# Performance work log

Hardware: AMD Instinct MI355X
Metric: run time of the kernel (lower is better)

Reference implementation:

```python
import jax, jax.numpy as jnp
import numpy as np

B, N, C = 8, 8192, 256
H, D, S = 8, 32, 32          # heads, dim_head, slice_num
HID = 4 * C                  # mlp hidden


def layernorm(x, w, b, eps=1e-5):
    mu = jnp.mean(x, axis=-1, keepdims=True)
    var = jnp.mean(jnp.square(x - mu), axis=-1, keepdims=True)
    return (x - mu) * jax.lax.rsqrt(var + eps) * w + b


def setup_inputs() -> dict:
    key = jax.random.key(0)
    ks = jax.random.split(key, 16)
    s = lambda fan: 1.0 / np.sqrt(fan)
    return {
        "fx": jax.random.normal(ks[0], (B, N, C), jnp.float32),
        "ln1_w": jnp.ones((C,), jnp.float32),
        "ln1_b": jnp.zeros((C,), jnp.float32),
        "Wx": jax.random.uniform(ks[1], (C, C), jnp.float32, -s(C), s(C)),   # in_project_x weight [inner,dim]
        "bx": jax.random.uniform(ks[2], (C,), jnp.float32, -s(C), s(C)),
        "Wq": jax.random.uniform(ks[3], (S, D), jnp.float32, -s(D), s(D)),
        "Wk": jax.random.uniform(ks[4], (S, D), jnp.float32, -s(D), s(D)),
        "Wv": jax.random.uniform(ks[5], (D, D), jnp.float32, -s(D), s(D)),
        "Wo": jax.random.uniform(ks[6], (C, C), jnp.float32, -s(C), s(C)),   # to_out weight [dim,inner]
        "bo": jax.random.uniform(ks[7], (C,), jnp.float32, -s(C), s(C)),
        "ln2_w": jnp.ones((C,), jnp.float32),
        "ln2_b": jnp.zeros((C,), jnp.float32),
        "W1": jax.random.uniform(ks[8], (HID, C), jnp.float32, -s(C), s(C)),
        "b1": jax.random.uniform(ks[9], (HID,), jnp.float32, -s(C), s(C)),
        "W2": jax.random.uniform(ks[10], (C, HID), jnp.float32, -s(HID), s(HID)),
        "b2": jax.random.uniform(ks[11], (C,), jnp.float32, -s(HID), s(HID)),
    }


def linear_no_attn(x, Wx, bx, Wq, Wk, Wv, Wo, bo):
    # x: [B,N,C]
    x_mid = x @ Wx.T + bx                                   # [B,N,C]
    x_mid = x_mid.reshape(x.shape[0], x.shape[1], H, D).transpose(0, 2, 1, 3)  # [B,H,N,D]
    q = jax.nn.softmax(x_mid @ Wq.T, axis=-1)               # [B,H,N,S], softmax over slices
    k = jax.nn.softmax(x_mid @ Wk.T, axis=-2)               # [B,H,N,S], softmax over tokens
    v = x_mid @ Wv.T                                        # [B,H,N,D]
    kv = jnp.einsum('bhns,bhnd->bhsd', k, v)                # [B,H,S,D]
    qkv = jnp.einsum('bhns,bhsd->bhnd', q, kv)              # [B,H,N,D]
    qkv = qkv.transpose(0, 2, 1, 3).reshape(x.shape[0], x.shape[1], H * D)
    return qkv @ Wo.T + bo


def reference(fx, ln1_w, ln1_b, Wx, bx, Wq, Wk, Wv, Wo, bo, ln2_w, ln2_b, W1, b1, W2, b2):
    h = linear_no_attn(layernorm(fx, ln1_w, ln1_b), Wx, bx, Wq, Wk, Wv, Wo, bo) + fx
    y = layernorm(h, ln2_w, ln2_b)
    y = jax.nn.gelu(y @ W1.T + b1, approximate=False)       # MLP: pre + exact GELU, n_layers=0
    y = y @ W2.T + b2
    return y + h
```

## Files before the change

kernel.cpp:

```cpp
#include <hip/hip_runtime.h>
#include <math.h>


typedef __attribute__((ext_vector_type(8))) short bf8;
typedef __attribute__((ext_vector_type(4))) float f32x4;
typedef __attribute__((ext_vector_type(4))) unsigned short u16x4;
typedef __attribute__((ext_vector_type(8))) unsigned short u16x8;

__device__ __forceinline__ float b2f(unsigned short x) {
  union { unsigned u; float f; } t; t.u = ((unsigned)x) << 16; return t.f;
}
__device__ __forceinline__ unsigned short f2b(float f) {
  union { float f; unsigned u; } t; t.f = f;
  unsigned r = t.u + 0x7fffu + ((t.u >> 16) & 1u);
  return (unsigned short)(r >> 16);
}
__device__ __forceinline__ float gelu_exact(float x) {
  return 0.5f * x * (1.0f + erff(x * 0.7071067811865475f));
}
__device__ __forceinline__ float erf_fast(float x) {
  float ax = fabsf(x);
  float t = __builtin_amdgcn_rcpf(fmaf(0.3275911f, ax, 1.0f));
  float p = t * fmaf(t, fmaf(t, fmaf(t, fmaf(t, 1.061405429f, -1.453152027f),
                                     1.421413741f), -0.284496736f), 0.254829592f);
  float r = 1.0f - p * __expf(-ax * ax);
  return copysignf(r, x);
}
__device__ __forceinline__ float gelu_fast(float x) {
  return 0.5f * x * (1.0f + erf_fast(x * 0.7071067811865475f));
}

typedef __attribute__((address_space(1))) const void gas_void;
typedef __attribute__((address_space(3))) void las_void;
__device__ __forceinline__ void gl_lds16(const void* g, void* l) {
  __builtin_amdgcn_global_load_lds((gas_void*)g, (las_void*)l, 16, 0, 0);
}

__global__ void sniff_kernel(const unsigned* __restrict__ fx, int* __restrict__ flag) {
  if (threadIdx.x == 0) {
    int cnt = 0;
    for (int i = 0; i < 64; i++) {
      unsigned e = (fx[i] >> 7) & 0xFFu;
      cnt += (e >= 117u && e <= 130u) ? 1 : 0;
    }
    *flag = (cnt >= 32) ? 1 : 0;
  }
}

struct CvtDesc { const void* src[15]; int off[15]; int n[15]; };

__global__ __launch_bounds__(256) void cvt_tab(CvtDesc d, unsigned short* __restrict__ wtab,
                                               const int* __restrict__ flagp) {
  const int seg = blockIdx.y;
  const int i = blockIdx.x * 256 + threadIdx.x;
  if (i >= d.n[seg]) return;
  unsigned short o;
  if (*flagp) o = ((const unsigned short*)d.src[seg])[i];
  else        o = f2b(((const float*)d.src[seg])[i]);
  wtab[d.off[seg] + i] = o;
}

__global__ __launch_bounds__(256) void build_big(
    const unsigned short* __restrict__ wq, const unsigned short* __restrict__ wk,
    unsigned short* __restrict__ Wqbig, unsigned short* __restrict__ Wkbig)
{
  const int idx = blockIdx.x * 256 + threadIdx.x;
  const int row = idx >> 8, col = idx & 255;
  const bool same = (row >> 5) == (col >> 5);
  const int wi = (row & 31) * 32 + (col & 31);
  Wqbig[idx] = same ? wq[wi] : (unsigned short)0;
  Wkbig[idx] = same ? wk[wi] : (unsigned short)0;
}

__global__ __launch_bounds__(256) void zero_u16(unsigned short* __restrict__ p, int n) {
  int i8 = (blockIdx.x * 256 + threadIdx.x) * 8;
  if (i8 < n) { u16x8 z = {}; *(u16x8*)&p[i8] = z; }
}

__global__ __launch_bounds__(256) void ln_stats(
    const void* __restrict__ X, const int* __restrict__ flagp, int amode,
    float* __restrict__ MU, float* __restrict__ RS)
{
  const int lane = threadIdx.x & 63;
  const int wave = threadIdx.x >> 6;
  const size_t row = (size_t)blockIdx.x * 4 + wave;
  const size_t base = row * 256 + lane * 4;
  const bool abf = amode ? ((*flagp) != 0) : true;
  float x0, x1, x2, x3;
  if (abf) {
    u16x4 uv = *(const u16x4*)&((const unsigned short*)X)[base];
    x0 = b2f(uv[0]); x1 = b2f(uv[1]); x2 = b2f(uv[2]); x3 = b2f(uv[3]);
  } else {
    f32x4 t = *(const f32x4*)&((const float*)X)[base];
    x0 = t[0]; x1 = t[1]; x2 = t[2]; x3 = t[3];
  }
  float s = x0 + x1 + x2 + x3;
  float q = x0*x0 + x1*x1 + x2*x2 + x3*x3;
  #pragma unroll
  for (int m = 1; m < 64; m <<= 1) { s += __shfl_xor(s, m, 64); q += __shfl_xor(q, m, 64); }
  float mean = s * (1.0f / 256.0f);
  float var  = q * (1.0f / 256.0f) - mean * mean;
  if (lane == 0) { MU[row] = mean; RS[row] = rsqrtf(var + 1e-5f); }
}

__global__ __launch_bounds__(256) void gemm_bt(
    const unsigned short* __restrict__ A,
    const unsigned short* __restrict__ W,
    const unsigned short* __restrict__ bias,
    const void* __restrict__ Res, const int* __restrict__ flagp,
    unsigned short* __restrict__ Y,
    int N, int K, int act, int mz, long wz)
{
  __shared__ __align__(16) unsigned short smem[3 * 8192];
  const int tid = threadIdx.x, lane = tid & 63, wave = tid >> 6;
  const size_t zrow = (size_t)blockIdx.z * mz;
  const int bm = blockIdx.x * 128, bn = blockIdx.y * 128;
  const int wm = (wave >> 1) * 64, wn = (wave & 1) * 64;
  const int quad = lane >> 4, l16 = lane & 15;
  const unsigned short* Wz = W + (size_t)blockIdx.z * wz;

  f32x4 acc[4][4] = {};
  const int r0 = tid >> 2;
  const int co = (tid & 3) * 8;
  const unsigned short* pa0 = &A[(zrow + bm + r0) * K + co];
  const unsigned short* pa1 = &A[(zrow + bm + r0 + 64) * K + co];
  const unsigned short* pb0 = &Wz[(size_t)(bn + r0) * K + co];
  const unsigned short* pb1 = &Wz[(size_t)(bn + r0 + 64) * K + co];
  const int nt = K >> 5;

  auto stage = [&](int t, int sl) {
    const int k0 = t << 5;
    unsigned short* b_ = &smem[sl * 8192 + tid * 8];
    gl_lds16(pa0 + k0, b_);
    gl_lds16(pa1 + k0, b_ + 2048);
    gl_lds16(pb0 + k0, b_ + 4096);
    gl_lds16(pb1 + k0, b_ + 6144);
  };

  stage(0, 0);
  if (nt > 1) stage(1, 1);
  int scur = 0, snew = 2;
  for (int t = 0; t < nt; ++t) {
    if (t + 2 < nt) {
      stage(t + 2, snew);
      asm volatile("s_waitcnt vmcnt(8)" ::: "memory");
    } else if (t + 1 < nt) {
      asm volatile("s_waitcnt vmcnt(4)" ::: "memory");
    } else {
      asm volatile("s_waitcnt vmcnt(0)" ::: "memory");
    }
    __builtin_amdgcn_s_barrier();
    __builtin_amdgcn_sched_barrier(0);

    const unsigned short* sa = &smem[scur * 8192];
    const unsigned short* sb = sa + 4096;
    bf8 af[4], bfr[4];
    #pragma unroll
    for (int i = 0; i < 4; i++) af[i]  = *(const bf8*)&sa[(wm + i * 16 + l16) * 32 + quad * 8];
    #pragma unroll
    for (int j = 0; j < 4; j++) bfr[j] = *(const bf8*)&sb[(wn + j * 16 + l16) * 32 + quad * 8];
    #pragma unroll
    for (int i = 0; i < 4; i++)
      #pragma unroll
      for (int j = 0; j < 4; j++)
        acc[i][j] = __builtin_amdgcn_mfma_f32_16x16x32_bf16(af[i], bfr[j], acc[i][j], 0, 0, 0);

    __builtin_amdgcn_sched_barrier(0);
    __builtin_amdgcn_s_barrier();
    scur = scur + 1 < 3 ? scur + 1 : 0;
    snew = snew + 1 < 3 ? snew + 1 : 0;
  }

  const bool rbf = Res ? ((*flagp) != 0) : true;
  float bv[4];
  #pragma unroll
  for (int j = 0; j < 4; j++) bv[j] = b2f(bias[bn + wn + j * 16 + l16]);
  #pragma unroll
  for (int i = 0; i < 4; i++)
    #pragma unroll
    for (int j = 0; j < 4; j++)
      #pragma unroll
      for (int r = 0; r < 4; r++) {
        float v = acc[i][j][r] + bv[j];
        if (act == 2) v = __expf(v);
        acc[i][j][r] = v;
      }
  if (act == 3) {
    #pragma unroll
    for (int i = 0; i < 4; i++)
      #pragma unroll
      for (int g = 0; g < 2; g++)
        #pragma unroll
        for (int r = 0; r < 4; r++) {
          float a0 = acc[i][2*g][r], a1 = acc[i][2*g+1][r];
          float m = fmaxf(a0, a1);
          #pragma unroll
          for (int msk = 1; msk < 16; msk <<= 1) m = fmaxf(m, __shfl_xor(m, msk, 64));
          float e0 = __expf(a0 - m), e1 = __expf(a1 - m);
          float s = e0 + e1;
          #pragma unroll
          for (int msk = 1; msk < 16; msk <<= 1) s += __shfl_xor(s, msk, 64);
          const float rz = 1.0f / s;
          acc[i][2*g][r] = e0 * rz; acc[i][2*g+1][r] = e1 * rz;
        }
  }

  float* cf = (float*)smem;
  const int whalf = wm >> 6;
  #pragma unroll
  for (int half = 0; half < 2; ++half) {
    __builtin_amdgcn_s_barrier();
    if (whalf == half) {
      #pragma unroll
      for (int i = 0; i < 4; i++)
        #pragma unroll
        for (int j = 0; j < 4; j++)
          #pragma unroll
          for (int r = 0; r < 4; r++)
            cf[(i * 16 + quad * 4 + r) * 132 + wn + j * 16 + l16] = acc[i][j][r];
    }
    __builtin_amdgcn_s_barrier();
    #pragma unroll
    for (int st = 0; st < 4; ++st) {
      const int e = st * 2048 + tid * 8;
      const int row = e >> 7;
      const int col = e & 127;
      const size_t gbase = (zrow + bm + half * 64 + row) * (size_t)N + bn + col;
      float v[8];
      #pragma unroll
      for (int u = 0; u < 8; u++) v[u] = cf[row * 132 + col + u];
      if (Res) {
        if (rbf) {
          u16x8 rv = *(const u16x8*)&((const unsigned short*)Res)[gbase];
          #pragma unroll
          for (int u = 0; u < 8; u++) v[u] += b2f(rv[u]);
        } else {
          f32x4 ra = *(const f32x4*)&((const float*)Res)[gbase];
          f32x4 rb = *(const f32x4*)&((const float*)Res)[gbase + 4];
          v[0] += ra[0]; v[1] += ra[1]; v[2] += ra[2]; v[3] += ra[3];
          v[4] += rb[0]; v[5] += rb[1]; v[6] += rb[2]; v[7] += rb[3];
        }
      }
      u16x8 o;
      #pragma unroll
      for (int u = 0; u < 8; u++) o[u] = f2b(v[u]);
      *(u16x8*)&Y[gbase] = o;
    }
  }
}

__global__ __launch_bounds__(256) void gemm_bt_ln(
    const void* __restrict__ A, const int* __restrict__ flagp, int amode,
    const float* __restrict__ MU, const float* __restrict__ RS,
    const unsigned short* __restrict__ lw, const unsigned short* __restrict__ lb,
    const unsigned short* __restrict__ W, const unsigned short* __restrict__ bias,
    unsigned short* __restrict__ Y, int N, int K, int act)
{
  __shared__ __align__(16) unsigned char smemc[32768];
  unsigned short* lA = (unsigned short*)smemc;
  unsigned short* lB = lA + 4096;
  const int tid = threadIdx.x, lane = tid & 63, wave = tid >> 6;
  const int bm = blockIdx.x * 128, bn = blockIdx.y * 128;
  const int wm = (wave >> 1) * 64, wn = (wave & 1) * 64;
  const int quad = lane >> 4, l16 = lane & 15;
  const bool abf = amode ? ((*flagp) != 0) : true;
  const unsigned short* Ab = (const unsigned short*)A;
  const float* Af = (const float*)A;

  f32x4 acc[4][4] = {};
  const int r0 = tid >> 2;
  const int co = (tid & 3) * 8;
  const unsigned short* pb0 = &W[(size_t)(bn + r0) * K + co];
  const unsigned short* pb1 = &W[(size_t)(bn + r0 + 64) * K + co];

  for (int k0 = 0; k0 < K; k0 += 32) {
    u16x8 wv8 = *(const u16x8*)&lw[k0 + co];
    u16x8 bv8 = *(const u16x8*)&lb[k0 + co];
    __syncthreads();
    gl_lds16(pb0 + k0, &lB[tid * 8]);
    gl_lds16(pb1 + k0, &lB[2048 + tid * 8]);
    #pragma unroll
    for (int half = 0; half < 2; half++) {
      const int ar = bm + r0 + half * 64;
      const float m_ = MU[ar], r_ = RS[ar];
      float xv[8];
      if (abf) {
        u16x8 t = *(const u16x8*)&Ab[(size_t)ar * K + k0 + co];
        #pragma unroll
        for (int e = 0; e < 8; e++) xv[e] = b2f(t[e]);
      } else {
        f32x4 t0 = *(const f32x4*)&Af[(size_t)ar * K + k0 + co];
        f32x4 t1 = *(const f32x4*)&Af[(size_t)ar * K + k0 + co + 4];
        xv[0]=t0[0]; xv[1]=t0[1]; xv[2]=t0[2]; xv[3]=t0[3];
        xv[4]=t1[0]; xv[5]=t1[1]; xv[6]=t1[2]; xv[7]=t1[3];
      }
      u16x8 o;
      #pragma unroll
      for (int e = 0; e < 8; e++)
        o[e] = f2b((xv[e] - m_) * r_ * b2f(wv8[e]) + b2f(bv8[e]));
      *(u16x8*)&lA[half * 2048 + tid * 8] = o;
    }
    __syncthreads();

    bf8 af[4], bfr[4];
    #pragma unroll
    for (int i = 0; i < 4; i++) af[i]  = *(const bf8*)&lA[(wm + i * 16 + l16) * 32 + quad * 8];
    #pragma unroll
    for (int j = 0; j < 4; j++) bfr[j] = *(const bf8*)&lB[(wn + j * 16 + l16) * 32 + quad * 8];
    #pragma unroll
    for (int i = 0; i < 4; i++)
      #pragma unroll
      for (int j = 0; j < 4; j++)
        acc[i][j] = __builtin_amdgcn_mfma_f32_16x16x32_bf16(af[i], bfr[j], acc[i][j], 0, 0, 0);
  }

  float bv[4];
  #pragma unroll
  for (int j = 0; j < 4; j++) bv[j] = b2f(bias[bn + wn + j * 16 + l16]);
  #pragma unroll
  for (int i = 0; i < 4; i++)
    #pragma unroll
    for (int j = 0; j < 4; j++)
      #pragma unroll
      for (int r = 0; r < 4; r++) {
        float v = acc[i][j][r] + bv[j];
        if (act) v = gelu_exact(v);
        acc[i][j][r] = v;
      }

  float* cf = (float*)smemc;
  const int whalf = wm >> 6;
  #pragma unroll
  for (int half = 0; half < 2; ++half) {
    __syncthreads();
    if (whalf == half) {
      #pragma unroll
      for (int i = 0; i < 4; i++)
        #pragma unroll
        for (int j = 0; j < 4; j++)
          #pragma unroll
          for (int r = 0; r < 4; r++)
            cf[(i * 16 + quad * 4 + r) * 128 + wn + j * 16 + l16] = acc[i][j][r];
    }
    __syncthreads();
    #pragma unroll
    for (int st = 0; st < 4; ++st) {
      const int e = st * 2048 + tid * 8;
      const int row = e >> 7;
      const size_t gbase = (size_t)(bm + half * 64 + row) * N + bn + (e & 127);
      u16x8 o;
      #pragma unroll
      for (int u = 0; u < 8; u++) o[u] = f2b(cf[e + u]);
      *(u16x8*)&Y[gbase] = o;
    }
  }
}

__global__ __launch_bounds__(256, 1) void fused_mlp(
    const unsigned short* __restrict__ Hsrc,
    const float* __restrict__ MU, const float* __restrict__ RS,
    const unsigned short* __restrict__ lw, const unsigned short* __restrict__ lb,
    const unsigned short* __restrict__ W1, const unsigned short* __restrict__ bs1,
    const unsigned short* __restrict__ W2, const unsigned short* __restrict__ bs2,
    void* __restrict__ OUT, const int* __restrict__ flagp, long row0)
{
  __shared__ __align__(16) unsigned char smem[77824];
  const int tid = threadIdx.x, lane = tid & 63, wave = tid >> 6;
  const int quad = lane >> 4, l16 = lane & 15;
  const int brow = blockIdx.x * 128;

  auto stageW1 = [&](int c, int b) {
    const unsigned short* src = W1 + (size_t)c * 8192;
    unsigned char* dst = smem + b * 16384;
    #pragma unroll
    for (int s = 0; s < 4; s++) {
      const int unit = s * 256 + tid;
      const int row = unit >> 5, u = unit & 31;
      gl_lds16(src + row * 256 + ((u ^ (row & 7)) * 8), dst + unit * 16);
    }
  };
  auto stageW2 = [&](int c, int b) {
    const unsigned short* src = W2 + c * 32;
    unsigned char* dst = smem + 32768 + b * 16384;
    #pragma unroll
    for (int s = 0; s < 4; s++) {
      const int unit = s * 256 + tid;
      const int row = unit >> 2, u = unit & 3;
      gl_lds16(src + (size_t)row * 1024 + ((u ^ ((row >> 1) & 3)) * 8), dst + unit * 16);
    }
  };

  stageW1(0, 0);
  stageW2(0, 0);

  unsigned short* b1l = (unsigned short*)(smem + 75776);
  if (tid < 128) *(u16x8*)&b1l[tid * 8] = *(const u16x8*)&bs1[tid * 8];

  bf8 areg[2][8];
  #pragma unroll
  for (int rg = 0; rg < 2; rg++) {
    const int myrow = wave * 32 + rg * 16 + l16;
    const float m_ = MU[brow + myrow], r_ = RS[brow + myrow];
    const unsigned short* hr = Hsrc + (size_t)(brow + myrow) * 256 + quad * 8;
    #pragma unroll
    for (int ks = 0; ks < 8; ks++) {
      u16x8 hv = *(const u16x8*)&hr[ks * 32];
      u16x8 wv = *(const u16x8*)&lw[ks * 32 + quad * 8];
      u16x8 bv = *(const u16x8*)&lb[ks * 32 + quad * 8];
      u16x8 o;
      #pragma unroll
      for (int e = 0; e < 8; e++)
        o[e] = f2b((b2f(hv[e]) - m_) * r_ * b2f(wv[e]) + b2f(bv[e]));
      *(u16x8*)&areg[rg][ks] = o;
    }
  }

  asm volatile("s_waitcnt vmcnt(0) lgkmcnt(0)" ::: "memory");
  __builtin_amdgcn_s_barrier();
  __builtin_amdgcn_sched_barrier(0);

  f32x4 acc[2][16] = {};
  unsigned short* tw = (unsigned short*)(smem + 65536 + wave * 2560);
  const int gsw = (l16 >> 1) & 3;
  int bsel = 0;

  for (int c = 0; c < 32; ++c) {
    if (c + 1 < 32) {
      stageW1(c + 1, bsel ^ 1);
      stageW2(c + 1, bsel ^ 1);
      __builtin_amdgcn_sched_barrier(0);
    }

    const unsigned short* w1b = (const unsigned short*)(smem + bsel * 16384);
    f32x4 p00 = {}, p01 = {}, p10 = {}, p11 = {};
    #pragma unroll
    for (int ks = 0; ks < 8; ks++) {
      const int slot = (ks * 4 + quad) ^ (l16 & 7);
      bf8 a0, a1;
      *(u16x8*)&a0 = *(const u16x8*)&w1b[l16 * 256 + slot * 8];
      *(u16x8*)&a1 = *(const u16x8*)&w1b[(16 + l16) * 256 + slot * 8];
      p00 = __builtin_amdgcn_mfma_f32_16x16x32_bf16(a0, areg[0][ks], p00, 0, 0, 0);
      p01 = __builtin_amdgcn_mfma_f32_16x16x32_bf16(a0, areg[1][ks], p01, 0, 0, 0);
      p10 = __builtin_amdgcn_mfma_f32_16x16x32_bf16(a1, areg[0][ks], p10, 0, 0, 0);
      p11 = __builtin_amdgcn_mfma_f32_16x16x32_bf16(a1, areg[1][ks], p11, 0, 0, 0);
    }

    {
      u16x4 bv0 = *(const u16x4*)&b1l[c * 32 + quad * 4];
      u16x4 bv1 = *(const u16x4*)&b1l[c * 32 + 16 + quad * 4];
      u16x4 o00, o01, o10, o11;
      #pragma unroll
      for (int r = 0; r < 4; r++) {
        o00[r] = f2b(gelu_fast(p00[r] + b2f(bv0[r])));
        o01[r] = f2b(gelu_fast(p01[r] + b2f(bv0[r])));
        o10[r] = f2b(gelu_fast(p10[r] + b2f(bv1[r])));
        o11[r] = f2b(gelu_fast(p11[r] + b2f(bv1[r])));
      }
      *(u16x4*)&tw[l16 * 40 + quad * 4]             = o00;
      *(u16x4*)&tw[(16 + l16) * 40 + quad * 4]      = o01;
      *(u16x4*)&tw[l16 * 40 + 16 + quad * 4]        = o10;
      *(u16x4*)&tw[(16 + l16) * 40 + 16 + quad * 4] = o11;
    }
    asm volatile("s_waitcnt lgkmcnt(0)" ::: "memory");
    __builtin_amdgcn_sched_barrier(0);

    bf8 ta0, ta1;
    *(u16x8*)&ta0 = *(const u16x8*)&tw[l16 * 40 + quad * 8];
    *(u16x8*)&ta1 = *(const u16x8*)&tw[(16 + l16) * 40 + quad * 8];
    const unsigned short* w2b = (const unsigned short*)(smem + 32768 + bsel * 16384);
    #pragma unroll
    for (int j = 0; j < 16; j++) {
      bf8 bw;
      *(u16x8*)&bw = *(const u16x8*)&w2b[(j * 16 + l16) * 32 + ((quad ^ gsw) * 8)];
      acc[0][j] = __builtin_amdgcn_mfma_f32_16x16x32_bf16(ta0, bw, acc[0][j], 0, 0, 0);
      acc[1][j] = __builtin_amdgcn_mfma_f32_16x16x32_bf16(ta1, bw, acc[1][j], 0, 0, 0);
    }

    asm volatile("s_waitcnt vmcnt(0)" ::: "memory");
    __builtin_amdgcn_s_barrier();
    __builtin_amdgcn_sched_barrier(0);
    bsel ^= 1;
  }

  const bool obf = (*flagp) != 0;
  float* cf = (float*)smem;
  #pragma unroll
  for (int h = 0; h < 2; ++h) {
    __syncthreads();
    if ((wave >> 1) == h) {
      const int wl = (wave & 1) * 32;
      #pragma unroll
      for (int rg = 0; rg < 2; rg++)
        #pragma unroll
        for (int j = 0; j < 16; j++)
          #pragma unroll
          for (int r = 0; r < 4; r++)
            cf[(wl + rg * 16 + quad * 4 + r) * 260 + j * 16 + l16] = acc[rg][j][r];
    }
    __syncthreads();
    const unsigned short* hrow = Hsrc + (size_t)(brow + h * 64) * 256;
    #pragma unroll
    for (int s = 0; s < 8; s++) {
      const int e = s * 2048 + tid * 8;
      const int row = e >> 8, col = e & 255;
      u16x8 rv = *(const u16x8*)&hrow[e];
      u16x8 b2v = *(const u16x8*)&bs2[col];
      float v[8];
      #pragma unroll
      for (int u = 0; u < 8; u++) v[u] = cf[row * 260 + col + u] + b2f(rv[u]) + b2f(b2v[u]);
      const size_t ob = (size_t)(row0 + brow + h * 64 + row) * 256 + col;
      if (obf) {
        u16x8 o;
        #pragma unroll
        for (int u = 0; u < 8; u++) o[u] = f2b(v[u]);
        *(u16x8*)&((unsigned short*)OUT)[ob] = o;
      } else {
        f32x4 oa, obv;
        oa[0]=v[0]; oa[1]=v[1]; oa[2]=v[2]; oa[3]=v[3];
        obv[0]=v[4]; obv[1]=v[5]; obv[2]=v[6]; obv[3]=v[7];
        *(f32x4*)&((float*)OUT)[ob] = oa;
        *(f32x4*)&((float*)OUT)[ob + 4] = obv;
      }
    }
  }
}

__global__ __launch_bounds__(256) void accumG(
    const unsigned short* __restrict__ X,
    const unsigned short* __restrict__ E,
    float* __restrict__ Gp)
{
  __shared__ float Xl[64 * 256];
  __shared__ __align__(16) unsigned short El[64 * 256];
  const int tid = threadIdx.x;
  const int k = blockIdx.x;
  const int h = tid >> 5, s = tid & 31;

  float acc[32];
  #pragma unroll
  for (int d = 0; d < 32; d++) acc[d] = 0.f;
  float zacc = 0.f;

  for (int sub = 0; sub < 4; sub++) {
    const size_t r0s = (size_t)k * 256 + sub * 64;
    __syncthreads();
    #pragma unroll
    for (int i = 0; i < 8; i++) {
      const int flat = i * 2048 + tid * 8;
      u16x8 xv = *(const u16x8*)&X[r0s * 256 + flat];
      #pragma unroll
      for (int e = 0; e < 8; e++) Xl[flat + e] = b2f(xv[e]);
      *(u16x8*)&El[flat] = *(const u16x8*)&E[r0s * 256 + flat];
    }
    __syncthreads();

    for (int t = 0; t < 64; t++) {
      const float e = b2f(El[t * 256 + h * 32 + s]);
      zacc += e;
      const int xb = t * 256 + h * 32;
      #pragma unroll
      for (int dq = 0; dq < 8; dq++) {
        f32x4 xv = *(const f32x4*)&Xl[xb + dq * 4];
        acc[dq*4+0] += e * xv[0];
        acc[dq*4+1] += e * xv[1];
        acc[dq*4+2] += e * xv[2];
        acc[dq*4+3] += e * xv[3];
      }
    }
  }

  float* gp = &Gp[(size_t)k * 8448 + (size_t)tid * 32];
  #pragma unroll
  for (int dq = 0; dq < 8; dq++) {
    f32x4 o; o[0]=acc[dq*4]; o[1]=acc[dq*4+1]; o[2]=acc[dq*4+2]; o[3]=acc[dq*4+3];
    *(f32x4*)&gp[dq * 4] = o;
  }
  Gp[(size_t)k * 8448 + 8192 + tid] = zacc;
}

__global__ __launch_bounds__(256) void reduceG(const float* __restrict__ Gp,
                                               float* __restrict__ Gfin) {
  const int o = blockIdx.x * 256 + threadIdx.x;
  if (o >= 67584) return;
  const int b = o / 8448;
  const int j = o - b * 8448;
  float s = 0.f;
  #pragma unroll 8
  for (int i = 0; i < 32; i++) s += Gp[(size_t)(b * 32 + i) * 8448 + j];
  Gfin[o] = s;
}

__global__ __launch_bounds__(256) void kv_build(
    const float* __restrict__ Gfin, const unsigned short* __restrict__ Wv,
    unsigned short* __restrict__ KVB)
{
  __shared__ float Gl[8192];
  __shared__ float zl[256];
  __shared__ float wvt[1024];
  const int tid = threadIdx.x;
  const int b = blockIdx.x;
  for (int i = tid; i < 8192; i += 256) Gl[i] = Gfin[(size_t)b * 8448 + i];
  zl[tid] = Gfin[(size_t)b * 8448 + 8192 + tid];
  for (int i = tid; i < 1024; i += 256) {
    const int dd = i >> 5, d = i & 31;
    wvt[i] = b2f(Wv[d * 32 + dd]);
  }
  __syncthreads();

  const int h = tid >> 5, d = tid & 31;
  unsigned short row[32];
  for (int s = 0; s < 32; s++) {
    float a = 0.f;
    #pragma unroll
    for (int dd = 0; dd < 32; dd++) a += Gl[h * 1024 + s * 32 + dd] * wvt[dd * 32 + d];
    row[s] = f2b(a / zl[h * 32 + s]);
  }
  unsigned short* out = &KVB[(size_t)b * 65536 + (size_t)(h * 32 + d) * 256 + h * 32];
  #pragma unroll
  for (int e = 0; e < 4; e++) *(u16x8*)&out[e * 8] = *(u16x8*)&row[e * 8];
}

__global__ __launch_bounds__(256) void copy_h0(const unsigned short* __restrict__ src,
                                               unsigned short* __restrict__ dst) {
  size_t i = ((size_t)blockIdx.x * 256 + threadIdx.x) * 8;
  *(u16x8*)&dst[i] = *(const u16x8*)&src[i];
}

extern "C" void kernel_launch(void* const* d_in, const int* in_sizes, int n_in,
                              void* d_out, int out_size, void* d_ws, size_t ws_size,
                              hipStream_t stream)
{
  const void* fx   = d_in[0];
  const void* ln1w = d_in[1];
  const void* ln1b = d_in[2];
  const void* Wx   = d_in[3];
  const void* bx   = d_in[4];
  const void* Wq   = d_in[5];
  const void* Wk   = d_in[6];
  const void* Wv   = d_in[7];
  const void* Wo   = d_in[8];
  const void* bo   = d_in[9];
  const void* ln2w = d_in[10];
  const void* ln2b = d_in[11];
  const void* W1   = d_in[12];
  const void* b1   = d_in[13];
  const void* W2   = d_in[14];
  const void* b2   = d_in[15];

  unsigned short* ws    = (unsigned short*)d_ws;
  unsigned short* hid   = ws;
  float* Gp             = (float*)ws;
  unsigned short* wtab  = ws + 8388608;
  unsigned short* h0res = wtab + 661248;
  float* Gfin           = (float*)h0res;
  unsigned short* Wqbig = h0res + 2097152;
  unsigned short* Wkbig = Wqbig + 65536;
  unsigned short* KVB   = Wkbig + 65536;
  unsigned short* zbias = KVB + 524288;
  float* fpw = (float*)(zbias + 256);
  float* mu1 = fpw;
  float* rs1 = fpw + 65536;
  float* mu2 = fpw + 131072;
  float* rs2 = fpw + 196608;
  int* flagp = (int*)(fpw + 262144);

  const int OFF_LN1W=0, OFF_LN1B=256, OFF_WX=512, OFF_BX=66048,
            OFF_WQ=66304, OFF_WK=67328, OFF_WV=68352,
            OFF_WO=69376, OFF_BO=134912, OFF_LN2W=135168, OFF_LN2B=135424,
            OFF_W1=135680, OFF_B1=397824, OFF_W2=398848, OFF_B2=660992;

  unsigned short* xm  = (unsigned short*)d_out;
  unsigned short* xup = xm + 16777216;

  sniff_kernel<<<1, 64, 0, stream>>>((const unsigned*)fx, flagp);
  CvtDesc cd;
  const void* srcs[15] = {ln1w, ln1b, Wx, bx, Wq, Wk, Wv, Wo, bo, ln2w, ln2b, W1, b1, W2, b2};
  const int offs[15]   = {OFF_LN1W, OFF_LN1B, OFF_WX, OFF_BX, OFF_WQ, OFF_WK, OFF_WV,
                          OFF_WO, OFF_BO, OFF_LN2W, OFF_LN2B, OFF_W1, OFF_B1, OFF_W2, OFF_B2};
  const int ns[15]     = {256, 256, 65536, 256, 1024, 1024, 1024, 65536, 256, 256, 256,
                          262144, 1024, 262144, 256};
  for (int i = 0; i < 15; i++) { cd.src[i] = srcs[i]; cd.off[i] = offs[i]; cd.n[i] = ns[i]; }
  cvt_tab<<<dim3(1024, 15), 256, 0, stream>>>(cd, wtab, flagp);
  build_big<<<256, 256, 0, stream>>>(wtab + OFF_WQ, wtab + OFF_WK, Wqbig, Wkbig);
  zero_u16<<<257, 256, 0, stream>>>(KVB, 524544);

  ln_stats<<<16384, 256, 0, stream>>>(fx, flagp, 1, mu1, rs1);
  gemm_bt_ln<<<dim3(512, 2), 256, 0, stream>>>(fx, flagp, 1, mu1, rs1,
      wtab + OFF_LN1W, wtab + OFF_LN1B, wtab + OFF_WX, wtab + OFF_BX,
      xm, 256, 256, 0);

  gemm_bt<<<dim3(512, 2), 256, 0, stream>>>(xm, Wkbig, zbias, nullptr, flagp,
                                            xup, 256, 256, 2, 0, 0);

  accumG<<<256, 256, 0, stream>>>(xm, xup, Gp);
  reduceG<<<264, 256, 0, stream>>>(Gp, Gfin);
  kv_build<<<8, 256, 0, stream>>>(Gfin, wtab + OFF_WV, KVB);

  gemm_bt<<<dim3(512, 2), 256, 0, stream>>>(xm, Wqbig, zbias, nullptr, flagp,
                                            xup, 256, 256, 3, 0, 0);

  gemm_bt<<<dim3(64, 2, 8), 256, 0, stream>>>(xup, KVB, zbias, nullptr, flagp,
                                              xm, 256, 256, 0, 8192, 65536);

  gemm_bt<<<dim3(512, 2), 256, 0, stream>>>(xm, wtab + OFF_WO, wtab + OFF_BO, fx, flagp,
                                            xup, 256, 256, 0, 0, 0);

  ln_stats<<<16384, 256, 0, stream>>>(xup, flagp, 0, mu2, rs2);
  copy_h0<<<4096, 256, 0, stream>>>(xup + (size_t)32768 * 256, hid);

  fused_mlp<<<256, 256, 0, stream>>>(xup, mu2, rs2,
      wtab + OFF_LN2W, wtab + OFF_LN2B, wtab + OFF_W1, wtab + OFF_B1,
      wtab + OFF_W2, wtab + OFF_B2, d_out, flagp, 0L);
  fused_mlp<<<256, 256, 0, stream>>>(hid, mu2 + 32768, rs2 + 32768,
      wtab + OFF_LN2W, wtab + OFF_LN2B, wtab + OFF_W1, wtab + OFF_B1,
      wtab + OFF_W2, wtab + OFF_B2, d_out, flagp, 32768L);
}
```

Measured before the change: 492.9 us.

## Merge two MLP launches into one grid with gated inter-block epilogue

Combines the two half-batch fused_mlp launches into a single 512-block launch, interleaving low and high halves. High-half blocks wait on a global atomic counter until all low-half blocks have written their outputs before running their epilogue, preserving the aliasing order. Launch bounds allow two blocks per CU to raise occupancy. This relies on all blocks being co-resident and may increase register pressure.

```diff
diff --git a/kernel.cpp b/kernel.cpp
--- a/kernel.cpp
+++ b/kernel.cpp
@@ -36,7 +36,8 @@
   __builtin_amdgcn_global_load_lds((gas_void*)g, (las_void*)l, 16, 0, 0);
 }
 
-__global__ void sniff_kernel(const unsigned* __restrict__ fx, int* __restrict__ flag) {
+__global__ void sniff_kernel(const unsigned* __restrict__ fx, int* __restrict__ flag,
+                             unsigned* __restrict__ gate) {
   if (threadIdx.x == 0) {
     int cnt = 0;
     for (int i = 0; i < 64; i++) {
@@ -44,6 +45,7 @@
       cnt += (e >= 117u && e <= 130u) ? 1 : 0;
     }
     *flag = (cnt >= 32) ? 1 : 0;
+    *gate = 0u;
   }
 }
 
@@ -356,18 +358,24 @@
   }
 }
 
-__global__ __launch_bounds__(256, 1) void fused_mlp(
-    const unsigned short* __restrict__ Hsrc,
+__global__ __launch_bounds__(256, 2) void fused_mlp(
+    const unsigned short* __restrict__ Hlo,
+    const unsigned short* __restrict__ Hhi,
     const float* __restrict__ MU, const float* __restrict__ RS,
     const unsigned short* __restrict__ lw, const unsigned short* __restrict__ lb,
     const unsigned short* __restrict__ W1, const unsigned short* __restrict__ bs1,
     const unsigned short* __restrict__ W2, const unsigned short* __restrict__ bs2,
-    void* __restrict__ OUT, const int* __restrict__ flagp, long row0)
+    void* __restrict__ OUT, const int* __restrict__ flagp,
+    unsigned* __restrict__ gate)
 {
   __shared__ __align__(16) unsigned char smem[77824];
   const int tid = threadIdx.x, lane = tid & 63, wave = tid >> 6;
   const int quad = lane >> 4, l16 = lane & 15;
-  const int brow = blockIdx.x * 128;
+  const int bid = blockIdx.x;
+  const bool low = (bid & 1) == 0;
+  const long grow = (low ? 0L : 32768L) + (long)(bid >> 1) * 128;
+  const unsigned short* hbase = low ? (Hlo + (size_t)grow * 256)
+                                    : (Hhi + ((size_t)grow - 32768) * 256);
 
   auto stageW1 = [&](int c, int b) {
     const unsigned short* src = W1 + (size_t)c * 8192;
@@ -400,8 +408,8 @@
   #pragma unroll
   for (int rg = 0; rg < 2; rg++) {
     const int myrow = wave * 32 + rg * 16 + l16;
-    const float m_ = MU[brow + myrow], r_ = RS[brow + myrow];
-    const unsigned short* hr = Hsrc + (size_t)(brow + myrow) * 256 + quad * 8;
+    const float m_ = MU[grow + myrow], r_ = RS[grow + myrow];
+    const unsigned short* hr = hbase + (size_t)myrow * 256 + quad * 8;
     #pragma unroll
     for (int ks = 0; ks < 8; ks++) {
       u16x8 hv = *(const u16x8*)&hr[ks * 32];
@@ -482,12 +490,20 @@
     bsel ^= 1;
   }
 
+  if (!low) {
+    if (tid == 0) {
+      while (__hip_atomic_load(gate, __ATOMIC_ACQUIRE, __HIP_MEMORY_SCOPE_AGENT) < 256u)
+        __builtin_amdgcn_s_sleep(32);
+    }
+    __syncthreads();
+  }
+
   const bool obf = (*flagp) != 0;
   float* cf = (float*)smem;
   #pragma unroll
-  for (int h = 0; h < 2; ++h) {
-    __syncthreads();
-    if ((wave >> 1) == h) {
+  for (int hh = 0; hh < 2; ++hh) {
+    __syncthreads();
+    if ((wave >> 1) == hh) {
       const int wl = (wave & 1) * 32;
       #pragma unroll
       for (int rg = 0; rg < 2; rg++)
@@ -498,7 +514,7 @@
             cf[(wl + rg * 16 + quad * 4 + r) * 260 + j * 16 + l16] = acc[rg][j][r];
     }
     __syncthreads();
-    const unsigned short* hrow = Hsrc + (size_t)(brow + h * 64) * 256;
+    const unsigned short* hrow = hbase + (size_t)(hh * 64) * 256;
     #pragma unroll
     for (int s = 0; s < 8; s++) {
       const int e = s * 2048 + tid * 8;
@@ -508,7 +524,7 @@
       float v[8];
       #pragma unroll
       for (int u = 0; u < 8; u++) v[u] = cf[row * 260 + col + u] + b2f(rv[u]) + b2f(b2v[u]);
-      const size_t ob = (size_t)(row0 + brow + h * 64 + row) * 256 + col;
+      const size_t ob = (size_t)(grow + hh * 64 + row) * 256 + col;
       if (obf) {
         u16x8 o;
         #pragma unroll
@@ -522,6 +538,12 @@
         *(f32x4*)&((float*)OUT)[ob + 4] = obv;
       }
     }
+  }
+
+  if (low) {
+    __syncthreads();
+    if (tid == 0)
+      __hip_atomic_fetch_add(gate, 1u, __ATOMIC_RELEASE, __HIP_MEMORY_SCOPE_AGENT);
   }
 }
 
@@ -663,6 +685,7 @@
   float* mu2 = fpw + 131072;
   float* rs2 = fpw + 196608;
   int* flagp = (int*)(fpw + 262144);
+  unsigned* gatep = (unsigned*)(flagp + 1);
 
   const int OFF_LN1W=0, OFF_LN1B=256, OFF_WX=512, OFF_BX=66048,
             OFF_WQ=66304, OFF_WK=67328, OFF_WV=68352,
@@ -672,7 +695,7 @@
   unsigned short* xm  = (unsigned short*)d_out;
   unsigned short* xup = xm + 16777216;
 
-  sniff_kernel<<<1, 64, 0, stream>>>((const unsigned*)fx, flagp);
+  sniff_kernel<<<1, 64, 0, stream>>>((const unsigned*)fx, flagp, gatep);
   CvtDesc cd;
   const void* srcs[15] = {ln1w, ln1b, Wx, bx, Wq, Wk, Wv, Wo, bo, ln2w, ln2b, W1, b1, W2, b2};
   const int offs[15]   = {OFF_LN1W, OFF_LN1B, OFF_WX, OFF_BX, OFF_WQ, OFF_WK, OFF_WV,
@@ -708,10 +731,7 @@
   ln_stats<<<16384, 256, 0, stream>>>(xup, flagp, 0, mu2, rs2);
   copy_h0<<<4096, 256, 0, stream>>>(xup + (size_t)32768 * 256, hid);
 
-  fused_mlp<<<256, 256, 0, stream>>>(xup, mu2, rs2,
+  fused_mlp<<<512, 256, 0, stream>>>(xup, hid, mu2, rs2,
       wtab + OFF_LN2W, wtab + OFF_LN2B, wtab + OFF_W1, wtab + OFF_B1,
-      wtab + OFF_W2, wtab + OFF_B2, d_out, flagp, 0L);
-  fused_mlp<<<256, 256, 0, stream>>>(hid, mu2 + 32768, rs2 + 32768,
-      wtab + OFF_LN2W, wtab + OFF_LN2B, wtab + OFF_W1, wtab + OFF_B1,
-      wtab + OFF_W2, wtab + OFF_B2, d_out, flagp, 32768L);
-}
+      wtab + OFF_W2, wtab + OFF_B2, d_out, flagp, gatep);
+}
```

After: 496.6 us. About the same (+0.7%).
